# Kernel optimization log

Hardware: AMD Instinct MI355X
Metric: run time of the kernel (lower is better)

The kernel has to match this reference:

```python
import math
import jax, jax.numpy as jnp
import numpy as np

NHEAD = 8


def setup_inputs() -> dict:
    key = jax.random.key(0)
    ks = jax.random.split(key, 16)
    B, S, M, Ss, Ksn, D = 8, 512, 8, 16, 16, 512
    f32 = jnp.float32
    w_scale = 0.05
    return {
        "q_temporal": jax.random.normal(ks[0], (B, S, M, D), f32),
        "k_temporal": jax.random.normal(ks[1], (B, S, M, D), f32),
        "v_temporal": jax.random.normal(ks[2], (B, S, M, D), f32),
        "q_static": jax.random.normal(ks[3], (B, Ss, D), f32),
        "k_static": jax.random.normal(ks[4], (B, Ksn, D), f32),
        "v_static": jax.random.normal(ks[5], (B, Ksn, D), f32),
        "mask_temporal": jax.random.randint(ks[6], (B, S, M), 0, 2).astype(jnp.int32),
        "mask_static": jax.random.randint(ks[7], (B, Ksn), 0, 2).astype(jnp.int32),
        "Wq": jax.random.normal(ks[8], (D, D), f32) * w_scale,
        "bq": jax.random.normal(ks[9], (D,), f32) * w_scale,
        "Wk": jax.random.normal(ks[10], (D, D), f32) * w_scale,
        "bk": jax.random.normal(ks[11], (D,), f32) * w_scale,
        "Wv": jax.random.normal(ks[12], (D, D), f32) * w_scale,
        "bv": jax.random.normal(ks[13], (D,), f32) * w_scale,
        "Wo": jax.random.normal(ks[14], (D, D), f32) * w_scale,
        "bo": jax.random.normal(ks[15], (D,), f32) * w_scale,
    }


def reference(q_temporal, k_temporal, v_temporal, q_static, k_static, v_static,
              mask_temporal, mask_static, Wq, bq, Wk, bk, Wv, bv, Wo, bo):
    B, S, M, D = q_temporal.shape
    dh = D // NHEAD
    scale = 1.0 / math.sqrt(dh)
    SM = S * M

    def lin(x, W, b):
        return x @ W + b

    def h5(x):  # [B,S,M,D] -> [B,H,S,M,dh]
        b, s, m, d = x.shape
        return x.reshape(b, s, m, NHEAD, dh).transpose(0, 3, 1, 2, 4)

    def h4(x):  # [B,N,D] -> [B,H,N,dh]
        b, n, d = x.shape
        return x.reshape(b, n, NHEAD, dh).transpose(0, 2, 1, 3)

    # additive masks: 1 -> 0 (keep), 0 -> -inf
    m_t = jnp.where(mask_temporal == 1, 0.0, -jnp.inf)  # [B,S,M]
    m_s = jnp.where(mask_static == 1, 0.0, -jnp.inf)    # [B,Ks]

    # shared static-key/value heads: [B,H,Ks,dh]
    Ks_h = h4(lin(k_static, Wk, bk))
    Vs_h = h4(lin(v_static, Wv, bv))

    # ---- temporal side ----
    Qt = h5(lin(q_temporal, Wq, bq))   # [B,H,S,M,dh]
    Kt = h5(lin(k_temporal, Wk, bk))
    Vt = h5(lin(v_temporal, Wv, bv))
    qt_kt = jnp.einsum('bhsmd,bhsnd->bhsmn', Qt, Kt) * scale + m_t[:, None, :, None, :]   # [B,H,S,M,M]
    qt_ks = jnp.einsum('bhsmd,bhkd->bhsmk', Qt, Ks_h) * scale + m_s[:, None, None, None, :]  # [B,H,S,M,Ks]
    w_t = jax.nn.softmax(jnp.concatenate([qt_kt, qt_ks], axis=-1), axis=-1)  # [B,H,S,M,M+Ks]
    qkv_t = (jnp.einsum('bhsmn,bhsnd->bhsmd', w_t[..., :M], Vt)
             + jnp.einsum('bhsmk,bhkd->bhsmd', w_t[..., M:], Vs_h))          # [B,H,S,M,dh]
    out_t = lin(qkv_t.transpose(0, 2, 3, 1, 4).reshape(B, S, M, D), Wo, bo)  # [B,S,M,D]

    # ---- static side ----
    Qs = h4(lin(q_static, Wq, bq))                              # [B,H,Ss,dh]
    Kt_f = h4(lin(k_temporal.reshape(B, SM, D), Wk, bk))        # [B,H,S*M,dh]
    Vt_f = h4(lin(v_temporal.reshape(B, SM, D), Wv, bv))
    qs_kt = jnp.einsum('bhqd,bhnd->bhqn', Qs, Kt_f) * scale + m_t.reshape(B, 1, 1, SM)  # [B,H,Ss,S*M]
    qs_ks = jnp.einsum('bhqd,bhkd->bhqk', Qs, Ks_h) * scale + m_s[:, None, None, :]     # [B,H,Ss,Ks]
    w_s = jax.nn.softmax(jnp.concatenate([qs_kt, qs_ks], axis=-1), axis=-1)  # [B,H,Ss,S*M+Ks]
    qkv_s = (jnp.einsum('bhqn,bhnd->bhqd', w_s[..., :SM], Vt_f)
             + jnp.einsum('bhqk,bhkd->bhqd', w_s[..., SM:], Vs_h))           # [B,H,Ss,dh]
    Ss = qkv_s.shape[2]
    out_s = lin(qkv_s.transpose(0, 2, 1, 3).reshape(B, Ss, D), Wo, bo)       # [B,Ss,D]

    return (out_t, w_t, out_s, w_s)
```

## Files before the change

kernel.cpp:

```cpp
#include <hip/hip_runtime.h>
#include <hip/hip_bf16.h>

typedef __attribute__((ext_vector_type(8))) __bf16 bf16x8;
typedef __attribute__((ext_vector_type(4))) float f32x4;

__device__ __forceinline__ float b2f(unsigned short u) {
    unsigned int x = ((unsigned int)u) << 16;
    float f;
    __builtin_memcpy(&f, &x, 4);
    return f;
}
__device__ __forceinline__ unsigned short f2b(float f) {
    __hip_bfloat16 h = __float2bfloat16(f);
    unsigned short u;
    __builtin_memcpy(&u, &h, 2);
    return u;
}
union U4 { uint4 v; unsigned short u[8]; };

__global__ __launch_bounds__(256) void transpose512cvt(const float* __restrict__ in,
                                                       unsigned short* __restrict__ out)
{
    __shared__ float tile[32][33];
    int tx = threadIdx.x & 31, ty = threadIdx.x >> 5;
    int bx = blockIdx.x, by = blockIdx.y;
    #pragma unroll
    for (int i = 0; i < 32; i += 8)
        tile[ty + i][tx] = in[(size_t)(bx * 32 + ty + i) * 512 + by * 32 + tx];
    __syncthreads();
    #pragma unroll
    for (int i = 0; i < 32; i += 8)
        out[(size_t)(by * 32 + ty + i) * 512 + bx * 32 + tx] = f2b(tile[tx][ty + i]);
}

#define GPAD 40

template<bool AF32, int CMODE>
__global__ __launch_bounds__(256) void gemm128(
    const void* __restrict__ Av,
    const unsigned short* __restrict__ Bt,
    const float* __restrict__ bias,
    void* __restrict__ Cv,
    int M, int N)
{
    const int K = 512;
    __shared__ __align__(16) unsigned short As[128 * GPAD];
    __shared__ __align__(16) unsigned short Bs[128 * GPAD];
    int m0 = blockIdx.x * 128, n0 = blockIdx.y * 128;
    int t = threadIdx.x;
    int wave = t >> 6, lane = t & 63, quad = lane >> 4, l16 = lane & 15;
    int wr = wave >> 1, wc = wave & 1;

    f32x4 acc[4][4];
    #pragma unroll
    for (int i = 0; i < 4; ++i)
        #pragma unroll
        for (int j = 0; j < 4; ++j) acc[i][j] = (f32x4){0.f, 0.f, 0.f, 0.f};

    int r = t >> 1, half = (t & 1) * 16;

    for (int k0 = 0; k0 < K; k0 += 32) {
        U4 a0, a1;
        uint4 b0, b1;
        if constexpr (AF32) {
            const float* Ap = (const float*)Av + (size_t)(m0 + r) * K + k0 + half;
            float4 f0 = ((const float4*)Ap)[0], f1 = ((const float4*)Ap)[1];
            float4 f2 = ((const float4*)Ap)[2], f3 = ((const float4*)Ap)[3];
            a0.u[0]=f2b(f0.x); a0.u[1]=f2b(f0.y); a0.u[2]=f2b(f0.z); a0.u[3]=f2b(f0.w);
            a0.u[4]=f2b(f1.x); a0.u[5]=f2b(f1.y); a0.u[6]=f2b(f1.z); a0.u[7]=f2b(f1.w);
            a1.u[0]=f2b(f2.x); a1.u[1]=f2b(f2.y); a1.u[2]=f2b(f2.z); a1.u[3]=f2b(f2.w);
            a1.u[4]=f2b(f3.x); a1.u[5]=f2b(f3.y); a1.u[6]=f2b(f3.z); a1.u[7]=f2b(f3.w);
        } else {
            const unsigned short* Ap = (const unsigned short*)Av + (size_t)(m0 + r) * K + k0 + half;
            a0.v = ((const uint4*)Ap)[0];
            a1.v = ((const uint4*)Ap)[1];
        }
        {
            const unsigned short* Bp = Bt + (size_t)(n0 + r) * K + k0 + half;
            b0 = ((const uint4*)Bp)[0];
            b1 = ((const uint4*)Bp)[1];
        }
        __syncthreads();
        *(uint4*)&As[r * GPAD + half] = a0.v;
        *(uint4*)&As[r * GPAD + half + 8] = a1.v;
        *(uint4*)&Bs[r * GPAD + half] = b0;
        *(uint4*)&Bs[r * GPAD + half + 8] = b1;
        __syncthreads();
        bf16x8 af[4], bf[4];
        #pragma unroll
        for (int i = 0; i < 4; ++i)
            af[i] = *(const bf16x8*)&As[(wr * 64 + i * 16 + l16) * GPAD + quad * 8];
        #pragma unroll
        for (int j = 0; j < 4; ++j)
            bf[j] = *(const bf16x8*)&Bs[(wc * 64 + j * 16 + l16) * GPAD + quad * 8];
        #pragma unroll
        for (int i = 0; i < 4; ++i)
            #pragma unroll
            for (int j = 0; j < 4; ++j)
                acc[i][j] = __builtin_amdgcn_mfma_f32_16x16x32_bf16(af[i], bf[j], acc[i][j], 0, 0, 0);
    }
    #pragma unroll
    for (int i = 0; i < 4; ++i) {
        #pragma unroll
        for (int j = 0; j < 4; ++j) {
            int row = m0 + wr * 64 + i * 16 + quad * 4;
            int col = n0 + wc * 64 + j * 16 + l16;
            float bc = bias[col];
            #pragma unroll
            for (int ii = 0; ii < 4; ++ii) {
                float v = acc[i][j][ii] + bc;
                int R = row + ii;
                if constexpr (CMODE == 0) {
                    ((float*)Cv)[(size_t)R * N + col] = v;
                } else if constexpr (CMODE == 1) {
                    ((unsigned short*)Cv)[(size_t)R * N + col] = f2b(v);
                } else {
                    int bb = R >> 12, n = R & 4095, hh = col >> 6, d = col & 63;
                    ((unsigned short*)Cv)[(((size_t)bb * 8 + hh) * 4096 + n) * 64 + d] = f2b(v);
                }
            }
        }
    }
}

__global__ __launch_bounds__(512) void temporal_attn(
    const unsigned short* __restrict__ Qt, const unsigned short* __restrict__ KH,
    const unsigned short* __restrict__ VH, const unsigned short* __restrict__ Ksp,
    const unsigned short* __restrict__ Vsp,
    const int* __restrict__ mask_t, const int* __restrict__ mask_s,
    float* __restrict__ w_t_out, unsigned short* __restrict__ qkv_t)
{
    int blk = blockIdx.x;
    int b = blk >> 8, sp = blk & 255;
    int s0 = sp * 2;
    int t = threadIdx.x;
    int h = t >> 6, lane = t & 63, quad = lane >> 4, l16 = lane & 15;

    __shared__ __align__(16) unsigned short Vt[8][64 * 40];
    __shared__ __align__(16) unsigned short Pl[8][16 * 40];

    size_t bh = (size_t)(b * 8 + h);
    size_t tok0 = ((size_t)(b * 512 + s0)) * 8;

    {
        int r = lane & 31, dh = (lane >> 5) * 32;
        const unsigned short* src = (r < 16)
            ? VH + (bh * 4096 + (size_t)(s0 * 8 + r)) * 64 + dh
            : Vsp + ((size_t)(b * 16 + (r - 16))) * 512 + h * 64 + dh;
        U4 u[4];
        #pragma unroll
        for (int g = 0; g < 4; ++g) u[g].v = ((const uint4*)src)[g];
        unsigned short* dst = &Vt[h][0];
        #pragma unroll
        for (int g = 0; g < 4; ++g)
            #pragma unroll
            for (int ii = 0; ii < 8; ++ii)
                dst[(dh + g * 8 + ii) * 40 + r] = u[g].u[ii];
    }

    const unsigned short* qp = Qt + (tok0 + l16) * 512 + h * 64 + quad * 8;
    bf16x8 qf0 = *(const bf16x8*)qp;
    bf16x8 qf1 = *(const bf16x8*)(qp + 32);
    const unsigned short* kpt = KH + (bh * 4096 + (size_t)(s0 * 8 + l16)) * 64 + quad * 8;
    bf16x8 kt0 = *(const bf16x8*)kpt;
    bf16x8 kt1 = *(const bf16x8*)(kpt + 32);
    const unsigned short* kps = Ksp + ((size_t)(b * 16 + l16)) * 512 + h * 64 + quad * 8;
    bf16x8 ks0 = *(const bf16x8*)kps;
    bf16x8 ks1 = *(const bf16x8*)(kps + 32);

    f32x4 sc0 = (f32x4){0.f, 0.f, 0.f, 0.f};
    f32x4 sc1 = (f32x4){0.f, 0.f, 0.f, 0.f};
    sc0 = __builtin_amdgcn_mfma_f32_16x16x32_bf16(qf0, kt0, sc0, 0, 0, 0);
    sc0 = __builtin_amdgcn_mfma_f32_16x16x32_bf16(qf1, kt1, sc0, 0, 0, 0);
    sc1 = __builtin_amdgcn_mfma_f32_16x16x32_bf16(qf0, ks0, sc1, 0, 0, 0);
    sc1 = __builtin_amdgcn_mfma_f32_16x16x32_bf16(qf1, ks1, sc1, 0, 0, 0);

    float madd0 = mask_t[tok0 + l16] ? 0.f : -1e30f;
    bool v0 = ((quad < 2) == (l16 < 8));
    if (!v0) madd0 = -1e30f;
    float madd1 = mask_s[b * 16 + l16] ? 0.f : -1e30f;

    float w0[4], w1[4];
    #pragma unroll
    for (int i = 0; i < 4; ++i) {
        float a = sc0[i] * 0.125f + madd0;
        float c = sc1[i] * 0.125f + madd1;
        float mx = fmaxf(a, c);
        mx = fmaxf(mx, __shfl_xor(mx, 1));
        mx = fmaxf(mx, __shfl_xor(mx, 2));
        mx = fmaxf(mx, __shfl_xor(mx, 4));
        mx = fmaxf(mx, __shfl_xor(mx, 8));
        float e0 = __expf(a - mx), e1 = __expf(c - mx);
        float se = e0 + e1;
        se += __shfl_xor(se, 1);
        se += __shfl_xor(se, 2);
        se += __shfl_xor(se, 4);
        se += __shfl_xor(se, 8);
        float inv = 1.f / se;
        w0[i] = e0 * inv;
        w1[i] = e1 * inv;
    }

    int row0 = quad * 4;
    #pragma unroll
    for (int i = 0; i < 4; ++i) {
        int row = row0 + i;
        Pl[h][row * 40 + l16] = f2b(w0[i]);
        Pl[h][row * 40 + 16 + l16] = f2b(w1[i]);
        int s = s0 + (row >> 3), m = row & 7;
        size_t wb = ((((size_t)b * 8 + h) * 512 + s) * 8 + m) * 24;
        if (v0) w_t_out[wb + (l16 & 7)] = w0[i];
        w_t_out[wb + 8 + l16] = w1[i];
    }

    bf16x8 pa = *(const bf16x8*)&Pl[h][l16 * 40 + quad * 8];
    f32x4 oacc[4];
    #pragma unroll
    for (int j = 0; j < 4; ++j) {
        bf16x8 vb = *(const bf16x8*)&Vt[h][(j * 16 + l16) * 40 + quad * 8];
        oacc[j] = (f32x4){0.f, 0.f, 0.f, 0.f};
        oacc[j] = __builtin_amdgcn_mfma_f32_16x16x32_bf16(pa, vb, oacc[j], 0, 0, 0);
    }
    #pragma unroll
    for (int j = 0; j < 4; ++j)
        #pragma unroll
        for (int ii = 0; ii < 4; ++ii) {
            int row = quad * 4 + ii;
            qkv_t[(tok0 + row) * 512 + h * 64 + j * 16 + l16] = f2b(oacc[j][ii]);
        }
}

__global__ __launch_bounds__(256) void static_attn_s1(
    const unsigned short* __restrict__ Qsp, const unsigned short* __restrict__ KH,
    const unsigned short* __restrict__ VH, const unsigned short* __restrict__ Ksp,
    const unsigned short* __restrict__ Vsp,
    const int* __restrict__ mask_t, const int* __restrict__ mask_s,
    float* __restrict__ w_s, float* __restrict__ Ppart, float* __restrict__ Lpart)
{
    int blk = blockIdx.x;
    int bh = blk & 63, c = blk >> 6;
    int b = bh >> 3, h = bh & 7;
    __shared__ __align__(16) unsigned short Klds[32 * 72];
    __shared__ __align__(16) unsigned short Vlds[64 * 40];
    __shared__ __align__(16) unsigned short Plds[16 * 40];
    __shared__ float maskv[32];
    __shared__ float sL[2][16];
    int t = threadIdx.x, wave = t >> 6, lane = t & 63, quad = lane >> 4, l16 = lane & 15;

    bf16x8 qf0 = *(const bf16x8*)(Qsp + ((size_t)(b * 16 + l16)) * 512 + h * 64 + quad * 8);
    bf16x8 qf1 = *(const bf16x8*)(Qsp + ((size_t)(b * 16 + l16)) * 512 + h * 64 + 32 + quad * 8);

    f32x4 pacc = (f32x4){0.f, 0.f, 0.f, 0.f};
    float Lacc[4] = {0.f, 0.f, 0.f, 0.f};
    int d0 = wave * 16;
    int sub = wave >> 1;
    int sr = t >> 3, spart = t & 7;
    int s0 = c * 16, s1 = (c == 7) ? 129 : (s0 + 16);

    for (int st = s0; st < s1; ++st) {
        int key0 = st * 32;
        int kk = key0 + sr;
        uint4 kv = {0, 0, 0, 0}, vv = {0, 0, 0, 0};
        if (kk < 4096) {
            kv = *(const uint4*)(KH + (((size_t)bh) * 4096 + kk) * 64 + spart * 8);
            vv = *(const uint4*)(VH + (((size_t)bh) * 4096 + kk) * 64 + spart * 8);
        } else if (kk < 4112) {
            kv = *(const uint4*)(Ksp + ((size_t)(b * 16 + kk - 4096)) * 512 + h * 64 + spart * 8);
            vv = *(const uint4*)(Vsp + ((size_t)(b * 16 + kk - 4096)) * 512 + h * 64 + spart * 8);
        }
        __syncthreads();
        *(uint4*)&Klds[sr * 72 + spart * 8] = kv;
        {
            U4 u; u.v = vv;
            #pragma unroll
            for (int ii = 0; ii < 8; ++ii) Vlds[(spart * 8 + ii) * 40 + sr] = u.u[ii];
        }
        if (t < 32) {
            int k2 = key0 + t;
            float ma = -1e30f;
            if (k2 < 4096) ma = mask_t[b * 4096 + k2] ? 0.f : -1e30f;
            else if (k2 < 4112) ma = mask_s[b * 16 + k2 - 4096] ? 0.f : -1e30f;
            maskv[t] = ma;
        }
        __syncthreads();
        if ((wave & 1) == 0) {
            bf16x8 kf0 = *(const bf16x8*)&Klds[(sub * 16 + l16) * 72 + quad * 8];
            bf16x8 kf1 = *(const bf16x8*)&Klds[(sub * 16 + l16) * 72 + 32 + quad * 8];
            f32x4 sc = (f32x4){0.f, 0.f, 0.f, 0.f};
            sc = __builtin_amdgcn_mfma_f32_16x16x32_bf16(qf0, kf0, sc, 0, 0, 0);
            sc = __builtin_amdgcn_mfma_f32_16x16x32_bf16(qf1, kf1, sc, 0, 0, 0);
            float ma = maskv[sub * 16 + l16];
            size_t wbase = (((size_t)bh) * 16 + quad * 4) * 4112 + key0 + sub * 16 + l16;
            #pragma unroll
            for (int i = 0; i < 4; ++i) {
                float sv = sc[i] * 0.125f + ma;
                float w = __expf(sv);
                Lacc[i] += w;
                w_s[wbase + (size_t)i * 4112] = w;
                Plds[(quad * 4 + i) * 40 + sub * 16 + l16] = f2b(w);
            }
        }
        __syncthreads();
        bf16x8 pf = *(const bf16x8*)&Plds[l16 * 40 + quad * 8];
        bf16x8 vf = *(const bf16x8*)&Vlds[(d0 + l16) * 40 + quad * 8];
        pacc = __builtin_amdgcn_mfma_f32_16x16x32_bf16(pf, vf, pacc, 0, 0, 0);
    }

    if ((wave & 1) == 0) {
        #pragma unroll
        for (int i = 0; i < 4; ++i) {
            float v = Lacc[i];
            v += __shfl_xor(v, 1);
            v += __shfl_xor(v, 2);
            v += __shfl_xor(v, 4);
            v += __shfl_xor(v, 8);
            Lacc[i] = v;
        }
        if (l16 == 0) {
            #pragma unroll
            for (int i = 0; i < 4; ++i) sL[wave >> 1][quad * 4 + i] = Lacc[i];
        }
    }
    size_t pbase = ((size_t)(bh * 8 + c) * 16 + quad * 4) * 64 + d0 + l16;
    #pragma unroll
    for (int i = 0; i < 4; ++i) Ppart[pbase + (size_t)i * 64] = pacc[i];
    __syncthreads();
    if (t < 16) Lpart[(bh * 8 + c) * 16 + t] = sL[0][t] + sL[1][t];
}

__global__ __launch_bounds__(256) void static_attn_s4(
    const float* __restrict__ Ppart, const float* __restrict__ Lpart,
    float* __restrict__ w_s, unsigned short* __restrict__ qkvS)
{
    int bh = blockIdx.x, b = bh >> 3, h = bh & 7;
    __shared__ float invL[16];
    int t = threadIdx.x;
    if (t < 16) {
        float L = 0.f;
        #pragma unroll
        for (int cc = 0; cc < 8; ++cc) L += Lpart[(bh * 8 + cc) * 16 + t];
        invL[t] = 1.f / L;
    }
    __syncthreads();
    #pragma unroll
    for (int i = 0; i < 4; ++i) {
        int idx = t + i * 256;
        int q = idx >> 6, d = idx & 63;
        float s = 0.f;
        #pragma unroll
        for (int cc = 0; cc < 8; ++cc) s += Ppart[((size_t)(bh * 8 + cc) * 16 + q) * 64 + d];
        qkvS[((size_t)(b * 16 + q)) * 512 + h * 64 + d] = f2b(s * invL[q]);
    }
    size_t base = (size_t)bh * 16 * 4112;
    for (int q = 0; q < 16; ++q) {
        float il = invL[q];
        for (int kk = t; kk < 4112; kk += 256) w_s[base + q * 4112 + kk] *= il;
    }
}

extern "C" void kernel_launch(void* const* d_in, const int* in_sizes, int n_in,
                              void* d_out, int out_size, void* d_ws, size_t ws_size,
                              hipStream_t stream)
{
    const float* q_t = (const float*)d_in[0];
    const float* k_t = (const float*)d_in[1];
    const float* v_t = (const float*)d_in[2];
    const float* q_s = (const float*)d_in[3];
    const float* k_s = (const float*)d_in[4];
    const float* v_s = (const float*)d_in[5];
    const int* m_t = (const int*)d_in[6];
    const int* m_s = (const int*)d_in[7];
    const float* Wq = (const float*)d_in[8];
    const float* bq = (const float*)d_in[9];
    const float* Wk = (const float*)d_in[10];
    const float* bk = (const float*)d_in[11];
    const float* Wv = (const float*)d_in[12];
    const float* bv = (const float*)d_in[13];
    const float* Wo = (const float*)d_in[14];
    const float* bo = (const float*)d_in[15];

    char* ws = (char*)d_ws;
    size_t off = 0;
    auto alloc = [&](size_t bytes) {
        void* p = ws + off;
        off += (bytes + 255) & ~(size_t)255;
        return p;
    };
    const size_t WB = (size_t)512 * 512 * 2;
    const size_t TB = (size_t)32768 * 512 * 2;
    const size_t SB = (size_t)128 * 512 * 2;
    unsigned short* WqT = (unsigned short*)alloc(WB);
    unsigned short* WkT = (unsigned short*)alloc(WB);
    unsigned short* WvT = (unsigned short*)alloc(WB);
    unsigned short* WoT = (unsigned short*)alloc(WB);
    unsigned short* Qt   = (unsigned short*)alloc(TB);
    unsigned short* KH   = (unsigned short*)alloc(TB);
    unsigned short* VH   = (unsigned short*)alloc(TB);
    unsigned short* qkvT = (unsigned short*)alloc(TB);
    unsigned short* Qsp  = (unsigned short*)alloc(SB);
    unsigned short* Ksp  = (unsigned short*)alloc(SB);
    unsigned short* Vsp  = (unsigned short*)alloc(SB);
    unsigned short* qkvS = (unsigned short*)alloc(SB);
    float* Ppart = (float*)alloc((size_t)64 * 8 * 16 * 64 * 4);
    float* Lpart = (float*)alloc((size_t)64 * 8 * 16 * 4);

    float* out    = (float*)d_out;
    float* out_tp = out;
    float* w_t_o  = out + 16777216;
    float* out_sp = out + 23068672;
    float* w_s_o  = out + 23134208;

    transpose512cvt<<<dim3(16, 16), 256, 0, stream>>>(Wq, WqT);
    transpose512cvt<<<dim3(16, 16), 256, 0, stream>>>(Wk, WkT);
    transpose512cvt<<<dim3(16, 16), 256, 0, stream>>>(Wv, WvT);
    transpose512cvt<<<dim3(16, 16), 256, 0, stream>>>(Wo, WoT);

    gemm128<true, 1><<<dim3(256, 4), 256, 0, stream>>>(q_t, WqT, bq, Qt, 32768, 512);
    gemm128<true, 2><<<dim3(256, 4), 256, 0, stream>>>(k_t, WkT, bk, KH, 32768, 512);
    gemm128<true, 2><<<dim3(256, 4), 256, 0, stream>>>(v_t, WvT, bv, VH, 32768, 512);
    gemm128<true, 1><<<dim3(1, 4),   256, 0, stream>>>(q_s, WqT, bq, Qsp, 128, 512);
    gemm128<true, 1><<<dim3(1, 4),   256, 0, stream>>>(k_s, WkT, bk, Ksp, 128, 512);
    gemm128<true, 1><<<dim3(1, 4),   256, 0, stream>>>(v_s, WvT, bv, Vsp, 128, 512);

    temporal_attn<<<2048, 512, 0, stream>>>(Qt, KH, VH, Ksp, Vsp, m_t, m_s, w_t_o, qkvT);
    static_attn_s1<<<512, 256, 0, stream>>>(Qsp, KH, VH, Ksp, Vsp, m_t, m_s, w_s_o, Ppart, Lpart);
    static_attn_s4<<<64, 256, 0, stream>>>(Ppart, Lpart, w_s_o, qkvS);

    gemm128<false, 0><<<dim3(256, 4), 256, 0, stream>>>(qkvT, WoT, bo, out_tp, 32768, 512);
    gemm128<false, 0><<<dim3(1, 4),   256, 0, stream>>>(qkvS, WoT, bo, out_sp, 128, 512);
}
```

Measured before the change: 599.5 us.

## Prefetch next K-tile into registers and swizzle GEMM blocks across XCDs

The GEMM kernel now issues global loads for the next K slice before running the MFMAs on the current slice, so load latency overlaps compute. The launch grid becomes 1D and block IDs are remapped so that blocks sharing the same A row-block are scheduled on the same XCD, which is meant to improve L2 reuse of the large f32 activation input. This adds register pressure from holding the prefetched f32 data, which could reduce occupancy.

```diff
diff --git a/kernel.cpp b/kernel.cpp
--- a/kernel.cpp
+++ b/kernel.cpp
@@ -46,7 +46,12 @@
     const int K = 512;
     __shared__ __align__(16) unsigned short As[128 * GPAD];
     __shared__ __align__(16) unsigned short Bs[128 * GPAD];
-    int m0 = blockIdx.x * 128, n0 = blockIdx.y * 128;
+
+    int nblk = gridDim.x, bid = blockIdx.x;
+    int wid = ((nblk & 7) == 0) ? ((bid & 7) * (nblk >> 3) + (bid >> 3)) : bid;
+    int nt = N >> 7;
+    int m0 = (wid / nt) * 128, n0 = (wid % nt) * 128;
+
     int t = threadIdx.x;
     int wave = t >> 6, lane = t & 63, quad = lane >> 4, l16 = lane & 15;
     int wr = wave >> 1, wc = wave & 1;
@@ -58,34 +63,47 @@
         for (int j = 0; j < 4; ++j) acc[i][j] = (f32x4){0.f, 0.f, 0.f, 0.f};
 
     int r = t >> 1, half = (t & 1) * 16;
-
-    for (int k0 = 0; k0 < K; k0 += 32) {
+    const float* Ap32 = (const float*)Av + (size_t)(m0 + r) * K + half;
+    const unsigned short* Ap16 = (const unsigned short*)Av + (size_t)(m0 + r) * K + half;
+    const unsigned short* Bp = Bt + (size_t)(n0 + r) * K + half;
+
+    float4 fa0, fa1, fa2, fa3;
+    U4 ua0, ua1;
+    uint4 fb0, fb1;
+
+    auto LOADK = [&](int k0) {
+        if constexpr (AF32) {
+            const float4* p = (const float4*)(Ap32 + k0);
+            fa0 = p[0]; fa1 = p[1]; fa2 = p[2]; fa3 = p[3];
+        } else {
+            ua0.v = *(const uint4*)(Ap16 + k0);
+            ua1.v = *(const uint4*)(Ap16 + k0 + 8);
+        }
+        fb0 = *(const uint4*)(Bp + k0);
+        fb1 = *(const uint4*)(Bp + k0 + 8);
+    };
+    auto STOREK = [&]() {
         U4 a0, a1;
-        uint4 b0, b1;
         if constexpr (AF32) {
-            const float* Ap = (const float*)Av + (size_t)(m0 + r) * K + k0 + half;
-            float4 f0 = ((const float4*)Ap)[0], f1 = ((const float4*)Ap)[1];
-            float4 f2 = ((const float4*)Ap)[2], f3 = ((const float4*)Ap)[3];
-            a0.u[0]=f2b(f0.x); a0.u[1]=f2b(f0.y); a0.u[2]=f2b(f0.z); a0.u[3]=f2b(f0.w);
-            a0.u[4]=f2b(f1.x); a0.u[5]=f2b(f1.y); a0.u[6]=f2b(f1.z); a0.u[7]=f2b(f1.w);
-            a1.u[0]=f2b(f2.x); a1.u[1]=f2b(f2.y); a1.u[2]=f2b(f2.z); a1.u[3]=f2b(f2.w);
-            a1.u[4]=f2b(f3.x); a1.u[5]=f2b(f3.y); a1.u[6]=f2b(f3.z); a1.u[7]=f2b(f3.w);
+            a0.u[0]=f2b(fa0.x); a0.u[1]=f2b(fa0.y); a0.u[2]=f2b(fa0.z); a0.u[3]=f2b(fa0.w);
+            a0.u[4]=f2b(fa1.x); a0.u[5]=f2b(fa1.y); a0.u[6]=f2b(fa1.z); a0.u[7]=f2b(fa1.w);
+            a1.u[0]=f2b(fa2.x); a1.u[1]=f2b(fa2.y); a1.u[2]=f2b(fa2.z); a1.u[3]=f2b(fa2.w);
+            a1.u[4]=f2b(fa3.x); a1.u[5]=f2b(fa3.y); a1.u[6]=f2b(fa3.z); a1.u[7]=f2b(fa3.w);
         } else {
-            const unsigned short* Ap = (const unsigned short*)Av + (size_t)(m0 + r) * K + k0 + half;
-            a0.v = ((const uint4*)Ap)[0];
-            a1.v = ((const uint4*)Ap)[1];
-        }
-        {
-            const unsigned short* Bp = Bt + (size_t)(n0 + r) * K + k0 + half;
-            b0 = ((const uint4*)Bp)[0];
-            b1 = ((const uint4*)Bp)[1];
-        }
-        __syncthreads();
+            a0 = ua0; a1 = ua1;
+        }
         *(uint4*)&As[r * GPAD + half] = a0.v;
         *(uint4*)&As[r * GPAD + half + 8] = a1.v;
-        *(uint4*)&Bs[r * GPAD + half] = b0;
-        *(uint4*)&Bs[r * GPAD + half + 8] = b1;
+        *(uint4*)&Bs[r * GPAD + half] = fb0;
+        *(uint4*)&Bs[r * GPAD + half + 8] = fb1;
+    };
+
+    LOADK(0);
+    for (int it = 0; it < 16; ++it) {
         __syncthreads();
+        STOREK();
+        __syncthreads();
+        if (it < 15) LOADK((it + 1) * 32);
         bf16x8 af[4], bf[4];
         #pragma unroll
         for (int i = 0; i < 4; ++i)
@@ -415,17 +433,17 @@
     transpose512cvt<<<dim3(16, 16), 256, 0, stream>>>(Wv, WvT);
     transpose512cvt<<<dim3(16, 16), 256, 0, stream>>>(Wo, WoT);
 
-    gemm128<true, 1><<<dim3(256, 4), 256, 0, stream>>>(q_t, WqT, bq, Qt, 32768, 512);
-    gemm128<true, 2><<<dim3(256, 4), 256, 0, stream>>>(k_t, WkT, bk, KH, 32768, 512);
-    gemm128<true, 2><<<dim3(256, 4), 256, 0, stream>>>(v_t, WvT, bv, VH, 32768, 512);
-    gemm128<true, 1><<<dim3(1, 4),   256, 0, stream>>>(q_s, WqT, bq, Qsp, 128, 512);
-    gemm128<true, 1><<<dim3(1, 4),   256, 0, stream>>>(k_s, WkT, bk, Ksp, 128, 512);
-    gemm128<true, 1><<<dim3(1, 4),   256, 0, stream>>>(v_s, WvT, bv, Vsp, 128, 512);
+    gemm128<true, 1><<<dim3(1024), 256, 0, stream>>>(q_t, WqT, bq, Qt, 32768, 512);
+    gemm128<true, 2><<<dim3(1024), 256, 0, stream>>>(k_t, WkT, bk, KH, 32768, 512);
+    gemm128<true, 2><<<dim3(1024), 256, 0, stream>>>(v_t, WvT, bv, VH, 32768, 512);
+    gemm128<true, 1><<<dim3(4),    256, 0, stream>>>(q_s, WqT, bq, Qsp, 128, 512);
+    gemm128<true, 1><<<dim3(4),    256, 0, stream>>>(k_s, WkT, bk, Ksp, 128, 512);
+    gemm128<true, 1><<<dim3(4),    256, 0, stream>>>(v_s, WvT, bv, Vsp, 128, 512);
 
     temporal_attn<<<2048, 512, 0, stream>>>(Qt, KH, VH, Ksp, Vsp, m_t, m_s, w_t_o, qkvT);
     static_attn_s1<<<512, 256, 0, stream>>>(Qsp, KH, VH, Ksp, Vsp, m_t, m_s, w_s_o, Ppart, Lpart);
     static_attn_s4<<<64, 256, 0, stream>>>(Ppart, Lpart, w_s_o, qkvS);
 
-    gemm128<false, 0><<<dim3(256, 4), 256, 0, stream>>>(qkvT, WoT, bo, out_tp, 32768, 512);
-    gemm128<false, 0><<<dim3(1, 4),   256, 0, stream>>>(qkvS, WoT, bo, out_sp, 128, 512);
-}
+    gemm128<false, 0><<<dim3(1024), 256, 0, stream>>>(qkvT, WoT, bo, out_tp, 32768, 512);
+    gemm128<false, 0><<<dim3(4),    256, 0, stream>>>(qkvS, WoT, bo, out_sp, 128, 512);
+}
```

After: 589.5 us. About the same (-1.7%).
